# Kernel tuning notes

Hardware: AMD Instinct MI355X
Metric: run time of the kernel (lower is better)

Reference implementation:

```python
import jax, jax.numpy as jnp
import numpy as np

NUM_USERS = 100000
NUM_ITEMS = 50000
NUM_NODES = NUM_USERS + NUM_ITEMS
EMBED_DIM = 64
NUM_LAYERS = 3
NUM_EDGES = 1000000


def setup_inputs() -> dict:
    key = jax.random.key(0)
    k_edge, k_emb = jax.random.split(key)
    edge_index = jax.random.randint(k_edge, (2, NUM_EDGES), 0, NUM_NODES, dtype=jnp.int64)
    # xavier_uniform for Embedding weight [N, d]
    limit = float(np.sqrt(6.0 / (NUM_NODES + EMBED_DIM)))
    emb = jax.random.uniform(k_emb, (NUM_NODES, EMBED_DIM), minval=-limit, maxval=limit, dtype=jnp.float32)
    alpha = jnp.full((NUM_LAYERS + 1,), 0.25, dtype=jnp.float32)
    return {"edge_index": edge_index, "emb": emb, "alpha": alpha}


def _gcn_norm(edge_index, num_nodes, dtype):
    # gcn_norm with add_self_loops=False, edge_weight = ones
    src, dst = edge_index[0], edge_index[1]
    w = jnp.ones((src.shape[0],), dtype=dtype)
    deg = jax.ops.segment_sum(w, dst, num_segments=num_nodes)  # degree at target
    deg_inv_sqrt = jnp.where(deg > 0, jax.lax.rsqrt(jnp.maximum(deg, 1e-30)), 0.0)
    return deg_inv_sqrt[src] * deg_inv_sqrt[dst]  # [E]


def get_embedding(emb, alpha, edge_index):
    src, dst = edge_index[0], edge_index[1]
    norm = _gcn_norm(edge_index, NUM_NODES, emb.dtype)  # [E]
    x = emb
    out = x * alpha[0]
    for i in range(NUM_LAYERS):
        # gather -> scale by edge norm -> scatter-add at target nodes
        msgs = norm[:, None] * x[src]                      # [E, d]
        x = jax.ops.segment_sum(msgs, dst, num_segments=NUM_NODES)  # [N, d]
        out = out + x * alpha[i + 1]
    return out


def reference(edge_index, emb, alpha):
    out = get_embedding(emb, alpha, edge_index)  # [N, d]
    out_src = out[edge_index[0]]                 # [E, d]
    out_dst = out[edge_index[1]]                 # [E, d]
    return jnp.sum(out_src * out_dst, axis=-1)   # [E]
```

## Files before the change

kernel.cpp:

```cpp
#include <hip/hip_runtime.h>
#include <hip/hip_fp16.h>

#define DIM 64
#define PCHUNK 2048
#define BSH 9
#define BNODES (1 << BSH)

__device__ __forceinline__ float2 h2f(unsigned int u) {
    __half2 h = *reinterpret_cast<__half2*>(&u);
    return __half22float2(h);
}
__device__ __forceinline__ unsigned int f2h(float a, float b) {
    __half2 h = __floats2half2_rn(a, b);
    return *reinterpret_cast<unsigned int*>(&h);
}

__device__ __forceinline__ bool edges_are_i64(const unsigned int* w) {
    unsigned int acc = 0;
#pragma unroll
    for (int k = 0; k < 8; ++k) acc |= w[2 * k + 1];
    return acc == 0;
}
__device__ __forceinline__ int ld_edge(const void* raw, bool is64, size_t idx) {
    return is64 ? (int)((const long long*)raw)[idx] : ((const int*)raw)[idx];
}

__global__ void k_partition(const void* ei_raw, int E, int NB, int CAP,
                            int* __restrict__ bwcnt, uint2* __restrict__ pe) {
    __shared__ int cnt[512], lstart[512], gb[512], lofs[512], psum[256];
    __shared__ uint2 stage[PCHUNK];
    __shared__ int gpos[PCHUNK];
    bool is64 = edges_are_i64((const unsigned int*)ei_raw);
    int base = blockIdx.x * PCHUNK;
    int n = E - base; if (n > PCHUNK) n = PCHUNK;
    int t = threadIdx.x;
    for (int b = t; b < 512; b += 256) { cnt[b] = 0; lofs[b] = 0; }
    __syncthreads();
    int s[8], d[8];
#pragma unroll
    for (int r = 0; r < 8; ++r) {
        int i = r * 256 + t;
        if (i < n) {
            s[r] = ld_edge(ei_raw, is64, (size_t)base + i);
            d[r] = ld_edge(ei_raw, is64, (size_t)E + base + i);
            atomicAdd(&cnt[d[r] >> BSH], 1);
        }
    }
    __syncthreads();
    int a0 = cnt[2 * t], a1 = cnt[2 * t + 1];
    psum[t] = a0 + a1;
    __syncthreads();
    int v = psum[t];
    for (int o = 1; o < 256; o <<= 1) {
        int tv = (t >= o) ? psum[t - o] : 0;
        __syncthreads();
        psum[t] += tv;
        __syncthreads();
    }
    int excl = psum[t] - v;
    lstart[2 * t] = excl;
    lstart[2 * t + 1] = excl + a0;
    __syncthreads();
    for (int b = t; b < NB; b += 256)
        if (cnt[b] > 0) gb[b] = atomicAdd(&bwcnt[b], cnt[b]);
    __syncthreads();
#pragma unroll
    for (int r = 0; r < 8; ++r) {
        int i = r * 256 + t;
        if (i < n) {
            int b = d[r] >> BSH;
            int j = atomicAdd(&lofs[b], 1);
            int slot = lstart[b] + j;
            stage[slot] = make_uint2((unsigned)s[r], (unsigned)d[r]);
            int gj = gb[b] + j;
            gpos[slot] = (gj < CAP) ? (b * CAP + gj) : (NB * CAP + slot);
        }
    }
    __syncthreads();
    for (int i = t; i < n; i += 256)
        pe[gpos[i]] = stage[i];
}

__global__ void k_bscan(const int* __restrict__ bwcnt, int* __restrict__ ebase, int NB) {
    __shared__ int sh[512];
    int tid = threadIdx.x;
    int v = (tid < NB) ? bwcnt[tid] : 0;
    sh[tid] = v;
    __syncthreads();
    for (int o = 1; o < 512; o <<= 1) {
        int t2 = (tid >= o) ? sh[tid - o] : 0;
        __syncthreads();
        sh[tid] += t2;
        __syncthreads();
    }
    if (tid < NB) ebase[tid] = sh[tid] - v;
    if (tid == NB - 1) ebase[NB] = sh[tid];
}

__global__ void k_bucket(const uint2* __restrict__ pe, const int* __restrict__ bwcnt,
                         const int* __restrict__ ebase, int CAP,
                         int* __restrict__ rowptr, float* __restrict__ dinv,
                         int* __restrict__ esrc, const float* __restrict__ emb,
                         __half* __restrict__ y0h, __half* __restrict__ embh,
                         int N, int E, int NB) {
    __shared__ int ldeg[BNODES], lcur[BNODES], psum[256];
    __shared__ float fdi[BNODES];
    int b = blockIdx.x;
    int n0 = b << BSH;
    int nn = N - n0; if (nn > BNODES) nn = BNODES;
    int ecnt = bwcnt[b];
    int eb = ebase[b];
    const uint2* win = pe + (size_t)b * CAP;
    int t = threadIdx.x;
    for (int j = t; j < BNODES; j += 256) ldeg[j] = 0;
    __syncthreads();
    for (int i = t; i < ecnt; i += 256)
        atomicAdd(&ldeg[win[i].y - n0], 1);
    __syncthreads();
    int a0 = ldeg[2 * t], a1 = ldeg[2 * t + 1];
    psum[t] = a0 + a1;
    __syncthreads();
    int v = psum[t];
    for (int o = 1; o < 256; o <<= 1) {
        int tv = (t >= o) ? psum[t - o] : 0;
        __syncthreads();
        psum[t] += tv;
        __syncthreads();
    }
    int excl = psum[t] - v;
    float d0 = a0 > 0 ? 1.0f / sqrtf((float)a0) : 0.0f;
    float d1 = a1 > 0 ? 1.0f / sqrtf((float)a1) : 0.0f;
    lcur[2 * t] = excl;
    lcur[2 * t + 1] = excl + a0;
    fdi[2 * t] = d0;
    fdi[2 * t + 1] = d1;
    if (2 * t < nn)     { rowptr[n0 + 2 * t] = eb + excl;          dinv[n0 + 2 * t] = d0; }
    if (2 * t + 1 < nn) { rowptr[n0 + 2 * t + 1] = eb + excl + a0; dinv[n0 + 2 * t + 1] = d1; }
    if (b == NB - 1 && t == 0) rowptr[N] = E;
    __syncthreads();
    for (int i = t; i < ecnt; i += 256) {
        uint2 rec = win[i];
        int pos = eb + atomicAdd(&lcur[rec.y - n0], 1);
        esrc[pos] = (int)rec.x;
    }
    for (int idx = t; idx < nn * 8; idx += 256) {
        int node = idx >> 3, c = idx & 7;
        float di = fdi[node];
        const float4* p = (const float4*)(emb + (size_t)(n0 + node) * DIM + c * 8);
        float4 a = p[0], bb = p[1];
        uint4 oy, oe;
        oy.x = f2h(di * a.x, di * a.y);   oy.y = f2h(di * a.z, di * a.w);
        oy.z = f2h(di * bb.x, di * bb.y); oy.w = f2h(di * bb.z, di * bb.w);
        oe.x = f2h(a.x, a.y);   oe.y = f2h(a.z, a.w);
        oe.z = f2h(bb.x, bb.y); oe.w = f2h(bb.z, bb.w);
        ((uint4*)(y0h + (size_t)(n0 + node) * DIM))[c] = oy;
        ((uint4*)(embh + (size_t)(n0 + node) * DIM))[c] = oe;
    }
}

__global__ void k_prop(const int* __restrict__ rowptr, const int* __restrict__ esrc,
                       const float* __restrict__ dinv, const __half* __restrict__ ycur,
                       __half* __restrict__ ynext, int N) {
    int t = blockIdx.x * blockDim.x + threadIdx.x;
    int node = t >> 3, c = t & 7;
    if (node >= N) return;
    int beg = rowptr[node], end = rowptr[node + 1];
    float acc[8] = {0.f, 0.f, 0.f, 0.f, 0.f, 0.f, 0.f, 0.f};
    for (int i = beg; i < end; ++i) {
        int s = esrc[i];
        uint4 u = ((const uint4*)(ycur + (size_t)s * DIM))[c];
        float2 f0 = h2f(u.x), f1 = h2f(u.y), f2 = h2f(u.z), f3 = h2f(u.w);
        acc[0] += f0.x; acc[1] += f0.y; acc[2] += f1.x; acc[3] += f1.y;
        acc[4] += f2.x; acc[5] += f2.y; acc[6] += f3.x; acc[7] += f3.y;
    }
    float di = dinv[node];
    float d2 = di * di;
    uint4 o;
    o.x = f2h(d2 * acc[0], d2 * acc[1]); o.y = f2h(d2 * acc[2], d2 * acc[3]);
    o.z = f2h(d2 * acc[4], d2 * acc[5]); o.w = f2h(d2 * acc[6], d2 * acc[7]);
    ((uint4*)(ynext + (size_t)node * DIM))[c] = o;
}

__global__ void k_outp(const int* __restrict__ rowptr, const int* __restrict__ esrc,
                       const float* __restrict__ dinv, const __half* __restrict__ y2h,
                       const __half* __restrict__ y1h, const __half* __restrict__ embh,
                       const float* __restrict__ alpha, __half* __restrict__ outh, int N) {
    int t = blockIdx.x * blockDim.x + threadIdx.x;
    int node = t >> 3, c = t & 7;
    if (node >= N) return;
    int beg = rowptr[node], end = rowptr[node + 1];
    float acc[8] = {0.f, 0.f, 0.f, 0.f, 0.f, 0.f, 0.f, 0.f};
    for (int i = beg; i < end; ++i) {
        int s = esrc[i];
        uint4 u = ((const uint4*)(y2h + (size_t)s * DIM))[c];
        float2 f0 = h2f(u.x), f1 = h2f(u.y), f2 = h2f(u.z), f3 = h2f(u.w);
        acc[0] += f0.x; acc[1] += f0.y; acc[2] += f1.x; acc[3] += f1.y;
        acc[4] += f2.x; acc[5] += f2.y; acc[6] += f3.x; acc[7] += f3.y;
    }
    float di = dinv[node];
    float sd = di > 0.f ? 1.0f / di : 0.0f;
    float a0 = alpha[0], a1 = alpha[1], a2 = alpha[2], a3 = alpha[3];
    uint4 ue = ((const uint4*)(embh + (size_t)node * DIM))[c];
    uint4 u1 = ((const uint4*)(y1h + (size_t)node * DIM))[c];
    uint4 u2 = ((const uint4*)(y2h + (size_t)node * DIM))[c];
    float2 e0 = h2f(ue.x), e1 = h2f(ue.y), e2 = h2f(ue.z), e3 = h2f(ue.w);
    float2 p0 = h2f(u1.x), p1 = h2f(u1.y), p2 = h2f(u1.z), p3 = h2f(u1.w);
    float2 q0 = h2f(u2.x), q1 = h2f(u2.y), q2 = h2f(u2.z), q3 = h2f(u2.w);
    float a3d = a3 * di;
    float o[8];
    o[0] = a0 * e0.x + sd * (a1 * p0.x + a2 * q0.x) + a3d * acc[0];
    o[1] = a0 * e0.y + sd * (a1 * p0.y + a2 * q0.y) + a3d * acc[1];
    o[2] = a0 * e1.x + sd * (a1 * p1.x + a2 * q1.x) + a3d * acc[2];
    o[3] = a0 * e1.y + sd * (a1 * p1.y + a2 * q1.y) + a3d * acc[3];
    o[4] = a0 * e2.x + sd * (a1 * p2.x + a2 * q2.x) + a3d * acc[4];
    o[5] = a0 * e2.y + sd * (a1 * p2.y + a2 * q2.y) + a3d * acc[5];
    o[6] = a0 * e3.x + sd * (a1 * p3.x + a2 * q3.x) + a3d * acc[6];
    o[7] = a0 * e3.y + sd * (a1 * p3.y + a2 * q3.y) + a3d * acc[7];
    uint4 u;
    u.x = f2h(o[0], o[1]); u.y = f2h(o[2], o[3]);
    u.z = f2h(o[4], o[5]); u.w = f2h(o[6], o[7]);
    ((uint4*)(outh + (size_t)node * DIM))[c] = u;
}

__global__ void k_final_h(const void* ei_raw, const __half* __restrict__ outh,
                          float* __restrict__ res, int E) {
    bool is64 = edges_are_i64((const unsigned int*)ei_raw);
    int t = blockIdx.x * blockDim.x + threadIdx.x;
    int e = t >> 3, c = t & 7;
    if (e >= E) return;
    int s = ld_edge(ei_raw, is64, (size_t)e);
    int d = ld_edge(ei_raw, is64, (size_t)E + e);
    uint4 ua = ((const uint4*)(outh + (size_t)s * DIM))[c];
    uint4 ub = ((const uint4*)(outh + (size_t)d * DIM))[c];
    float2 a0 = h2f(ua.x), a1 = h2f(ua.y), a2 = h2f(ua.z), a3 = h2f(ua.w);
    float2 b0 = h2f(ub.x), b1 = h2f(ub.y), b2 = h2f(ub.z), b3 = h2f(ub.w);
    float p = a0.x * b0.x + a0.y * b0.y + a1.x * b1.x + a1.y * b1.y +
              a2.x * b2.x + a2.y * b2.y + a3.x * b3.x + a3.y * b3.y;
    p += __shfl_down(p, 4, 8);
    p += __shfl_down(p, 2, 8);
    p += __shfl_down(p, 1, 8);
    if (c == 0) res[e] = p;
}

static inline size_t alignUp(size_t x) { return (x + 511) & ~size_t(511); }

extern "C" void kernel_launch(void* const* d_in, const int* in_sizes, int n_in,
                              void* d_out, int out_size, void* d_ws, size_t ws_size,
                              hipStream_t stream) {
    const void*  ei    = d_in[0];
    const float* emb   = (const float*)d_in[1];
    const float* alpha = (const float*)d_in[2];
    float*       res   = (float*)d_out;

    const int E = in_sizes[0] / 2;
    const int N = in_sizes[1] / DIM;

    const int NB = (N + BNODES - 1) >> BSH;
    int cap = (E / NB) * 3 / 2;
    const int CAP = (cap + 1023) & ~1023;

    char* w = (char*)d_ws;
    size_t off = 0;
    int*    bwcnt  = (int*)(w + off);    off = alignUp(off + (size_t)(NB + 1) * sizeof(int));
    int*    ebase  = (int*)(w + off);    off = alignUp(off + (size_t)(NB + 1) * sizeof(int));
    float*  dinv   = (float*)(w + off);  off = alignUp(off + (size_t)N * sizeof(float));
    int*    rowptr = (int*)(w + off);    off = alignUp(off + (size_t)(N + 1) * sizeof(int));
    int*    esrc   = (int*)(w + off);    off = alignUp(off + (size_t)E * sizeof(int));
    uint2*  pe     = (uint2*)(w + off);  off = alignUp(off + ((size_t)NB * CAP + PCHUNK) * sizeof(uint2));
    __half* y0h    = (__half*)(w + off); off = alignUp(off + (size_t)N * DIM * sizeof(__half));
    __half* y1h    = (__half*)(w + off); off = alignUp(off + (size_t)N * DIM * sizeof(__half));
    __half* y2h    = (__half*)(w + off); off = alignUp(off + (size_t)N * DIM * sizeof(__half));
    __half* embh   = (__half*)(w + off); off = alignUp(off + (size_t)N * DIM * sizeof(__half));
    __half* outh   = (__half*)(w + off); off = alignUp(off + (size_t)N * DIM * sizeof(__half));
    (void)ws_size;

    const int B = 256;

    hipMemsetAsync(bwcnt, 0, (size_t)(NB + 1) * sizeof(int), stream);

    int npart = (E + PCHUNK - 1) / PCHUNK;
    k_partition<<<npart, 256, 0, stream>>>(ei, E, NB, CAP, bwcnt, pe);
    k_bscan<<<1, 512, 0, stream>>>(bwcnt, ebase, NB);
    k_bucket<<<NB, 256, 0, stream>>>(pe, bwcnt, ebase, CAP, rowptr, dinv, esrc,
                                     emb, y0h, embh, N, E, NB);

    long long tN8 = (long long)N * 8;
    int ggrid = (int)((tN8 + B - 1) / B);
    k_prop<<<ggrid, B, 0, stream>>>(rowptr, esrc, dinv, y0h, y1h, N);
    k_prop<<<ggrid, B, 0, stream>>>(rowptr, esrc, dinv, y1h, y2h, N);
    k_outp<<<ggrid, B, 0, stream>>>(rowptr, esrc, dinv, y2h, y1h, embh, alpha, outh, N);

    long long tE8 = (long long)E * 8;
    k_final_h<<<(int)((tE8 + B - 1) / B), B, 0, stream>>>(ei, outh, res, E);
}
```

Baseline: 183.4 us.

## Fold bucket scan into k_bucket, unroll gathers, cache int32 edge list

```diff
diff --git a/kernel.cpp b/kernel.cpp
--- a/kernel.cpp
+++ b/kernel.cpp
@@ -26,7 +26,8 @@
 }
 
 __global__ void k_partition(const void* ei_raw, int E, int NB, int CAP,
-                            int* __restrict__ bwcnt, uint2* __restrict__ pe) {
+                            int* __restrict__ bwcnt, uint2* __restrict__ pe,
+                            int* __restrict__ edges32) {
     __shared__ int cnt[512], lstart[512], gb[512], lofs[512], psum[256];
     __shared__ uint2 stage[PCHUNK];
     __shared__ int gpos[PCHUNK];
@@ -43,6 +44,8 @@
         if (i < n) {
             s[r] = ld_edge(ei_raw, is64, (size_t)base + i);
             d[r] = ld_edge(ei_raw, is64, (size_t)E + base + i);
+            edges32[base + i] = s[r];
+            edges32[E + base + i] = d[r];
             atomicAdd(&cnt[d[r] >> BSH], 1);
         }
     }
@@ -81,39 +84,34 @@
         pe[gpos[i]] = stage[i];
 }
 
-__global__ void k_bscan(const int* __restrict__ bwcnt, int* __restrict__ ebase, int NB) {
-    __shared__ int sh[512];
-    int tid = threadIdx.x;
-    int v = (tid < NB) ? bwcnt[tid] : 0;
-    sh[tid] = v;
-    __syncthreads();
-    for (int o = 1; o < 512; o <<= 1) {
-        int t2 = (tid >= o) ? sh[tid - o] : 0;
-        __syncthreads();
-        sh[tid] += t2;
-        __syncthreads();
-    }
-    if (tid < NB) ebase[tid] = sh[tid] - v;
-    if (tid == NB - 1) ebase[NB] = sh[tid];
-}
-
 __global__ void k_bucket(const uint2* __restrict__ pe, const int* __restrict__ bwcnt,
-                         const int* __restrict__ ebase, int CAP,
-                         int* __restrict__ rowptr, float* __restrict__ dinv,
+                         int CAP, int* __restrict__ rowptr, float* __restrict__ dinv,
                          int* __restrict__ esrc, const float* __restrict__ emb,
                          __half* __restrict__ y0h, __half* __restrict__ embh,
                          int N, int E, int NB) {
     __shared__ int ldeg[BNODES], lcur[BNODES], psum[256];
     __shared__ float fdi[BNODES];
+    __shared__ int s_eb;
     int b = blockIdx.x;
     int n0 = b << BSH;
     int nn = N - n0; if (nn > BNODES) nn = BNODES;
     int ecnt = bwcnt[b];
-    int eb = ebase[b];
     const uint2* win = pe + (size_t)b * CAP;
     int t = threadIdx.x;
+    int part = 0;
+    for (int j = t; j < b; j += 256) part += bwcnt[j];
+    psum[t] = part;
+    __syncthreads();
+    for (int o = 1; o < 256; o <<= 1) {
+        int tv = (t >= o) ? psum[t - o] : 0;
+        __syncthreads();
+        psum[t] += tv;
+        __syncthreads();
+    }
+    if (t == 255) s_eb = psum[255];
     for (int j = t; j < BNODES; j += 256) ldeg[j] = 0;
     __syncthreads();
+    int eb = s_eb;
     for (int i = t; i < ecnt; i += 256)
         atomicAdd(&ldeg[win[i].y - n0], 1);
     __syncthreads();
@@ -158,6 +156,12 @@
     }
 }
 
+__device__ __forceinline__ void acc_row(float* acc, uint4 u) {
+    float2 f0 = h2f(u.x), f1 = h2f(u.y), f2 = h2f(u.z), f3 = h2f(u.w);
+    acc[0] += f0.x; acc[1] += f0.y; acc[2] += f1.x; acc[3] += f1.y;
+    acc[4] += f2.x; acc[5] += f2.y; acc[6] += f3.x; acc[7] += f3.y;
+}
+
 __global__ void k_prop(const int* __restrict__ rowptr, const int* __restrict__ esrc,
                        const float* __restrict__ dinv, const __half* __restrict__ ycur,
                        __half* __restrict__ ynext, int N) {
@@ -166,12 +170,19 @@
     if (node >= N) return;
     int beg = rowptr[node], end = rowptr[node + 1];
     float acc[8] = {0.f, 0.f, 0.f, 0.f, 0.f, 0.f, 0.f, 0.f};
-    for (int i = beg; i < end; ++i) {
+    int i = beg;
+    for (; i + 3 < end; i += 4) {
+        int s0 = esrc[i], s1 = esrc[i + 1], s2 = esrc[i + 2], s3 = esrc[i + 3];
+        uint4 u0 = ((const uint4*)(ycur + (size_t)s0 * DIM))[c];
+        uint4 u1 = ((const uint4*)(ycur + (size_t)s1 * DIM))[c];
+        uint4 u2 = ((const uint4*)(ycur + (size_t)s2 * DIM))[c];
+        uint4 u3 = ((const uint4*)(ycur + (size_t)s3 * DIM))[c];
+        acc_row(acc, u0); acc_row(acc, u1); acc_row(acc, u2); acc_row(acc, u3);
+    }
+    for (; i < end; ++i) {
         int s = esrc[i];
         uint4 u = ((const uint4*)(ycur + (size_t)s * DIM))[c];
-        float2 f0 = h2f(u.x), f1 = h2f(u.y), f2 = h2f(u.z), f3 = h2f(u.w);
-        acc[0] += f0.x; acc[1] += f0.y; acc[2] += f1.x; acc[3] += f1.y;
-        acc[4] += f2.x; acc[5] += f2.y; acc[6] += f3.x; acc[7] += f3.y;
+        acc_row(acc, u);
     }
     float di = dinv[node];
     float d2 = di * di;
@@ -190,22 +201,29 @@
     if (node >= N) return;
     int beg = rowptr[node], end = rowptr[node + 1];
     float acc[8] = {0.f, 0.f, 0.f, 0.f, 0.f, 0.f, 0.f, 0.f};
-    for (int i = beg; i < end; ++i) {
+    int i = beg;
+    for (; i + 3 < end; i += 4) {
+        int s0 = esrc[i], s1 = esrc[i + 1], s2 = esrc[i + 2], s3 = esrc[i + 3];
+        uint4 u0 = ((const uint4*)(y2h + (size_t)s0 * DIM))[c];
+        uint4 u1 = ((const uint4*)(y2h + (size_t)s1 * DIM))[c];
+        uint4 u2 = ((const uint4*)(y2h + (size_t)s2 * DIM))[c];
+        uint4 u3 = ((const uint4*)(y2h + (size_t)s3 * DIM))[c];
+        acc_row(acc, u0); acc_row(acc, u1); acc_row(acc, u2); acc_row(acc, u3);
+    }
+    for (; i < end; ++i) {
         int s = esrc[i];
         uint4 u = ((const uint4*)(y2h + (size_t)s * DIM))[c];
-        float2 f0 = h2f(u.x), f1 = h2f(u.y), f2 = h2f(u.z), f3 = h2f(u.w);
-        acc[0] += f0.x; acc[1] += f0.y; acc[2] += f1.x; acc[3] += f1.y;
-        acc[4] += f2.x; acc[5] += f2.y; acc[6] += f3.x; acc[7] += f3.y;
+        acc_row(acc, u);
     }
     float di = dinv[node];
     float sd = di > 0.f ? 1.0f / di : 0.0f;
     float a0 = alpha[0], a1 = alpha[1], a2 = alpha[2], a3 = alpha[3];
     uint4 ue = ((const uint4*)(embh + (size_t)node * DIM))[c];
-    uint4 u1 = ((const uint4*)(y1h + (size_t)node * DIM))[c];
-    uint4 u2 = ((const uint4*)(y2h + (size_t)node * DIM))[c];
+    uint4 u1v = ((const uint4*)(y1h + (size_t)node * DIM))[c];
+    uint4 u2v = ((const uint4*)(y2h + (size_t)node * DIM))[c];
     float2 e0 = h2f(ue.x), e1 = h2f(ue.y), e2 = h2f(ue.z), e3 = h2f(ue.w);
-    float2 p0 = h2f(u1.x), p1 = h2f(u1.y), p2 = h2f(u1.z), p3 = h2f(u1.w);
-    float2 q0 = h2f(u2.x), q1 = h2f(u2.y), q2 = h2f(u2.z), q3 = h2f(u2.w);
+    float2 p0 = h2f(u1v.x), p1 = h2f(u1v.y), p2 = h2f(u1v.z), p3 = h2f(u1v.w);
+    float2 q0 = h2f(u2v.x), q1 = h2f(u2v.y), q2 = h2f(u2v.z), q3 = h2f(u2v.w);
     float a3d = a3 * di;
     float o[8];
     o[0] = a0 * e0.x + sd * (a1 * p0.x + a2 * q0.x) + a3d * acc[0];
@@ -222,14 +240,13 @@
     ((uint4*)(outh + (size_t)node * DIM))[c] = u;
 }
 
-__global__ void k_final_h(const void* ei_raw, const __half* __restrict__ outh,
+__global__ void k_final_h(const int* __restrict__ edges32, const __half* __restrict__ outh,
                           float* __restrict__ res, int E) {
-    bool is64 = edges_are_i64((const unsigned int*)ei_raw);
     int t = blockIdx.x * blockDim.x + threadIdx.x;
     int e = t >> 3, c = t & 7;
     if (e >= E) return;
-    int s = ld_edge(ei_raw, is64, (size_t)e);
-    int d = ld_edge(ei_raw, is64, (size_t)E + e);
+    int s = edges32[e];
+    int d = edges32[E + e];
     uint4 ua = ((const uint4*)(outh + (size_t)s * DIM))[c];
     uint4 ub = ((const uint4*)(outh + (size_t)d * DIM))[c];
     float2 a0 = h2f(ua.x), a1 = h2f(ua.y), a2 = h2f(ua.z), a3 = h2f(ua.w);
@@ -261,17 +278,17 @@
 
     char* w = (char*)d_ws;
     size_t off = 0;
-    int*    bwcnt  = (int*)(w + off);    off = alignUp(off + (size_t)(NB + 1) * sizeof(int));
-    int*    ebase  = (int*)(w + off);    off = alignUp(off + (size_t)(NB + 1) * sizeof(int));
-    float*  dinv   = (float*)(w + off);  off = alignUp(off + (size_t)N * sizeof(float));
-    int*    rowptr = (int*)(w + off);    off = alignUp(off + (size_t)(N + 1) * sizeof(int));
-    int*    esrc   = (int*)(w + off);    off = alignUp(off + (size_t)E * sizeof(int));
-    uint2*  pe     = (uint2*)(w + off);  off = alignUp(off + ((size_t)NB * CAP + PCHUNK) * sizeof(uint2));
-    __half* y0h    = (__half*)(w + off); off = alignUp(off + (size_t)N * DIM * sizeof(__half));
-    __half* y1h    = (__half*)(w + off); off = alignUp(off + (size_t)N * DIM * sizeof(__half));
-    __half* y2h    = (__half*)(w + off); off = alignUp(off + (size_t)N * DIM * sizeof(__half));
-    __half* embh   = (__half*)(w + off); off = alignUp(off + (size_t)N * DIM * sizeof(__half));
-    __half* outh   = (__half*)(w + off); off = alignUp(off + (size_t)N * DIM * sizeof(__half));
+    int*    bwcnt   = (int*)(w + off);    off = alignUp(off + (size_t)(NB + 1) * sizeof(int));
+    float*  dinv    = (float*)(w + off);  off = alignUp(off + (size_t)N * sizeof(float));
+    int*    rowptr  = (int*)(w + off);    off = alignUp(off + (size_t)(N + 1) * sizeof(int));
+    int*    esrc    = (int*)(w + off);    off = alignUp(off + (size_t)E * sizeof(int));
+    int*    edges32 = (int*)(w + off);    off = alignUp(off + (size_t)2 * E * sizeof(int));
+    uint2*  pe      = (uint2*)(w + off);  off = alignUp(off + ((size_t)NB * CAP + PCHUNK) * sizeof(uint2));
+    __half* y0h     = (__half*)(w + off); off = alignUp(off + (size_t)N * DIM * sizeof(__half));
+    __half* y1h     = (__half*)(w + off); off = alignUp(off + (size_t)N * DIM * sizeof(__half));
+    __half* y2h     = (__half*)(w + off); off = alignUp(off + (size_t)N * DIM * sizeof(__half));
+    __half* embh    = (__half*)(w + off); off = alignUp(off + (size_t)N * DIM * sizeof(__half));
+    __half* outh    = (__half*)(w + off); off = alignUp(off + (size_t)N * DIM * sizeof(__half));
     (void)ws_size;
 
     const int B = 256;
@@ -279,9 +296,8 @@
     hipMemsetAsync(bwcnt, 0, (size_t)(NB + 1) * sizeof(int), stream);
 
     int npart = (E + PCHUNK - 1) / PCHUNK;
-    k_partition<<<npart, 256, 0, stream>>>(ei, E, NB, CAP, bwcnt, pe);
-    k_bscan<<<1, 512, 0, stream>>>(bwcnt, ebase, NB);
-    k_bucket<<<NB, 256, 0, stream>>>(pe, bwcnt, ebase, CAP, rowptr, dinv, esrc,
+    k_partition<<<npart, 256, 0, stream>>>(ei, E, NB, CAP, bwcnt, pe, edges32);
+    k_bucket<<<NB, 256, 0, stream>>>(pe, bwcnt, CAP, rowptr, dinv, esrc,
                                      emb, y0h, embh, N, E, NB);
 
     long long tN8 = (long long)N * 8;
@@ -291,5 +307,5 @@
     k_outp<<<ggrid, B, 0, stream>>>(rowptr, esrc, dinv, y2h, y1h, embh, alpha, outh, N);
 
     long long tE8 = (long long)E * 8;
-    k_final_h<<<(int)((tE8 + B - 1) / B), B, 0, stream>>>(ei, outh, res, E);
-}
+    k_final_h<<<(int)((tE8 + B - 1) / B), B, 0, stream>>>(edges32, outh, res, E);
+}
```

Result: faster. 162.5 us (-11.4%).
